# Kernel optimization log

Hardware: AMD Instinct MI355X
Metric: run time of the kernel (lower is better)

## Reference

```python
import jax, jax.numpy as jnp
import numpy as np

NUM_EXPERTS = 8
IN_FEATURES = 1024
OUT_FEATURES = 1024
TOTAL_TOKENS = 8192


def setup_inputs() -> dict:
    key = jax.random.key(0)
    k_x, k_w, k_b = jax.random.split(key, 3)
    inputs = jax.random.normal(k_x, (TOTAL_TOKENS, IN_FEATURES), dtype=jnp.float32)
    # lecun_normal-style scale for the per-expert kernels
    kernel = jax.random.normal(k_w, (NUM_EXPERTS, IN_FEATURES, OUT_FEATURES), dtype=jnp.float32) / np.sqrt(IN_FEATURES)
    bias = jax.random.normal(k_b, (NUM_EXPERTS, OUT_FEATURES), dtype=jnp.float32) * 0.01
    # ragged group sizes that sum exactly to TOTAL_TOKENS (tokens pre-sorted by expert)
    rng = np.random.default_rng(0)
    gs = rng.multinomial(TOTAL_TOKENS, [1.0 / NUM_EXPERTS] * NUM_EXPERTS)
    group_sizes = jnp.asarray(gs, dtype=jnp.int32)
    return {"inputs": inputs, "group_sizes": group_sizes, "kernel": kernel, "bias": bias}


def reference(inputs, group_sizes, kernel, bias):
    # inputs: [T, in], kernel: [E, in, out], bias: [E, out], group_sizes: [E]
    E = kernel.shape[0]
    T = inputs.shape[0]
    # per-token expert id (tokens are sorted/grouped by expert)
    expert_ids = jnp.repeat(jnp.arange(E, dtype=jnp.int32), group_sizes, total_repeat_length=T)  # [T]
    onehot = jax.nn.one_hot(expert_ids, E, dtype=inputs.dtype)  # [T, E]
    # grouped ragged matmul: y[t] = x[t] @ W[expert_ids[t]]
    xe = jnp.einsum("te,ti->eti", onehot, inputs)  # [E, T, in], zero outside each expert's group
    y = jnp.einsum("eti,eio->to", xe, kernel)  # [T, out]
    # ragged bias expansion: bias of the owning expert per token
    y = y + jnp.take(bias, expert_ids, axis=0)
    return y
```

## Files before the change

### kernel.cpp

```cpp
#include <hip/hip_runtime.h>
#include <hip/hip_bf16.h>

#define KDIM 1024
#define NDIM 1024
#define NEXP 8
#define TTOK 8192

typedef __bf16 bf16x8 __attribute__((ext_vector_type(8)));
typedef __bf16 bf16x4 __attribute__((ext_vector_type(4)));
typedef float  f32x4  __attribute__((ext_vector_type(4)));

__device__ __forceinline__ void gl2lds16(const void* g, void* l) {
  __builtin_amdgcn_global_load_lds(
      (const __attribute__((address_space(1))) void*)g,
      (__attribute__((address_space(3))) void*)l, 16, 0, 0);
}

__global__ __launch_bounds__(256) void prepass(
    const float* __restrict__ x, const float* __restrict__ W,
    __bf16* __restrict__ xb, __bf16* __restrict__ Wt)
{
  __shared__ __align__(16) __bf16 Lt[64 * 72];
  const int t = threadIdx.x;
  if (blockIdx.x < 1024) {
    int gid = blockIdx.x * 256 + t;
#pragma unroll
    for (int p = 0; p < 4; ++p) {
      size_t i8 = (size_t)(gid + p * 262144) * 8;
      float4 a = *(const float4*)(x + i8);
      float4 b = *(const float4*)(x + i8 + 4);
      bf16x8 v;
      v[0] = (__bf16)a.x; v[1] = (__bf16)a.y; v[2] = (__bf16)a.z; v[3] = (__bf16)a.w;
      v[4] = (__bf16)b.x; v[5] = (__bf16)b.y; v[6] = (__bf16)b.z; v[7] = (__bf16)b.w;
      *(bf16x8*)(xb + i8) = v;
    }
  } else {
    int bid = blockIdx.x - 1024;
    int e = bid >> 8, r = bid & 255;
    int k0 = (r >> 4) * 64, n0 = (r & 15) * 64;
    const float* Wp = W + (size_t)e * KDIM * NDIM;
    int rr0 = t >> 4, c4 = t & 15;
#pragma unroll
    for (int p = 0; p < 4; ++p) {
      int kk = rr0 + p * 16;
      float4 v = *(const float4*)(Wp + (size_t)(k0 + kk) * NDIM + n0 + c4 * 4);
      Lt[(c4 * 4 + 0) * 72 + kk] = (__bf16)v.x;
      Lt[(c4 * 4 + 1) * 72 + kk] = (__bf16)v.y;
      Lt[(c4 * 4 + 2) * 72 + kk] = (__bf16)v.z;
      Lt[(c4 * 4 + 3) * 72 + kk] = (__bf16)v.w;
    }
    __syncthreads();
    __bf16* Wte = Wt + (size_t)e * NDIM * KDIM;
    int n = t >> 2, kq = t & 3;
#pragma unroll
    for (int q = 0; q < 2; ++q) {
      int kqq = kq + q * 4;
      bf16x8 v = *(const bf16x8*)(Lt + n * 72 + kqq * 8);
      *(bf16x8*)(Wte + (size_t)(n0 + n) * KDIM + k0 + kqq * 8) = v;
    }
  }
}

__global__ __launch_bounds__(256) void moe_gemm_bf16(
    const __bf16* __restrict__ xb, const __bf16* __restrict__ Wt,
    const int* __restrict__ gs, const float* __restrict__ bias,
    float* __restrict__ out)
{
  __shared__ __align__(16) __bf16 Al0[4096], Bl0[4096];
  __shared__ __align__(16) __bf16 Al1[4096], Bl1[4096];

  int y = blockIdx.y;
  int e = 0, row0 = 0, rows = 0, found = 0, off = 0;
#pragma unroll
  for (int i = 0; i < NEXP; ++i) {
    int g = gs[i];
    int tc = (g + 127) >> 7;
    if (!found) {
      if (y < tc) { found = 1; e = i; row0 = off + y * 128; rows = min(128, g - y * 128); }
      else y -= tc;
    }
    off += g;
  }
  if (!found) return;
  const int n0 = blockIdx.x * 128;

  const int t = threadIdx.x, lane = t & 63, wv = t >> 6;
  const int wm = wv & 1, wn = wv >> 1, lm = lane & 15, lg = lane >> 4;

  const int c0 = wv * 2, c1 = wv * 2 + 1;
  const int s0 = c0 * 64 + lane, s1 = c1 * 64 + lane;
  const int r0 = s0 & 127, k0h = s0 >> 7;
  const int r1 = s1 & 127, k1h = s1 >> 7;

  const __bf16* gA0 = xb + (size_t)(row0 + r0) * KDIM + k0h * 8;
  const __bf16* gA1 = xb + (size_t)(row0 + r1) * KDIM + k1h * 8;
  const __bf16* Wte = Wt + (size_t)e * NDIM * KDIM;
  const __bf16* gB0 = Wte + (size_t)(n0 + r0) * KDIM + k0h * 8;
  const __bf16* gB1 = Wte + (size_t)(n0 + r1) * KDIM + k1h * 8;

  f32x4 acc[4][4] = {};

  auto stage = [&](int kt, __bf16* lA, __bf16* lB) {
    const int ko = kt * 32;
    gl2lds16(gA0 + ko, lA + c0 * 512);
    gl2lds16(gA1 + ko, lA + c1 * 512);
    gl2lds16(gB0 + ko, lB + c0 * 512);
    gl2lds16(gB1 + ko, lB + c1 * 512);
  };

  auto compute = [&](const __bf16* lA, const __bf16* lB) {
    bf16x8 af[4], bfr[4];
#pragma unroll
    for (int i = 0; i < 4; ++i)
      af[i] = *(const bf16x8*)(lA + lg * 1024 + (wm * 64 + i * 16 + lm) * 8);
#pragma unroll
    for (int j = 0; j < 4; ++j)
      bfr[j] = *(const bf16x8*)(lB + lg * 1024 + (wn * 64 + j * 16 + lm) * 8);
#pragma unroll
    for (int i = 0; i < 4; ++i)
#pragma unroll
      for (int j = 0; j < 4; ++j)
        acc[i][j] = __builtin_amdgcn_mfma_f32_16x16x32_bf16(af[i], bfr[j], acc[i][j], 0, 0, 0);
  };

  stage(0, Al0, Bl0);
#pragma unroll 1
  for (int kt = 0; kt < KDIM / 32; kt += 2) {
    __syncthreads();
    stage(kt + 1, Al1, Bl1);
    compute(Al0, Bl0);
    __syncthreads();
    if (kt + 2 < KDIM / 32) stage(kt + 2, Al0, Bl0);
    compute(Al1, Bl1);
  }

  float bj[4];
#pragma unroll
  for (int j = 0; j < 4; ++j) bj[j] = bias[e * NDIM + n0 + wn * 64 + j * 16 + lm];
  float* op = out + (size_t)row0 * NDIM + n0;
#pragma unroll
  for (int i = 0; i < 4; ++i)
#pragma unroll
    for (int r = 0; r < 4; ++r) {
      int rr = wm * 64 + i * 16 + lg * 4 + r;
      if (rr < rows) {
#pragma unroll
        for (int j = 0; j < 4; ++j)
          op[(size_t)rr * NDIM + wn * 64 + j * 16 + lm] = acc[i][j][r] + bj[j];
      }
    }
}

#define LDA 40
__global__ __launch_bounds__(256) void moe_gemm_kernel(
    const float* __restrict__ x, const int* __restrict__ gs,
    const float* __restrict__ W, const float* __restrict__ bias,
    float* __restrict__ out)
{
  __shared__ __bf16 Al[128 * LDA];
  __shared__ __bf16 Bl[128 * LDA];
  const int e = blockIdx.z, mt = blockIdx.y, nt = blockIdx.x;
  int off = 0;
#pragma unroll
  for (int i = 0; i < NEXP; ++i) { int g = gs[i]; if (i < e) off += g; }
  const int ge = gs[e];
  const int m0 = mt * 128;
  if (m0 >= ge) return;
  const int rows = min(128, ge - m0);
  const int row0 = off + m0;
  const int n0 = nt * 128;
  const int t = threadIdx.x, lane = t & 63, wv = t >> 6;
  const int wm = wv & 1, wn = wv >> 1, lm = lane & 15, lg = lane >> 4;
  const int am = t >> 3, kq = t & 7, nb = t & 127, kh = t >> 7;
  float4 aReg[4]; float bReg[16];
  const float* Wp = W + (size_t)e * KDIM * NDIM + n0 + nb;
  auto load_tile = [&](int kt) {
#pragma unroll
    for (int p = 0; p < 4; ++p) {
      int r = am + 32 * p;
      if (r < rows) aReg[p] = *(const float4*)(x + (size_t)(row0 + r) * KDIM + kt * 32 + kq * 4);
      else aReg[p] = make_float4(0.f, 0.f, 0.f, 0.f);
    }
    const float* wp = Wp + (size_t)(kt * 32 + kh * 16) * NDIM;
#pragma unroll
    for (int j = 0; j < 16; ++j) bReg[j] = wp[(size_t)j * NDIM];
  };
  auto store_tile = [&]() {
#pragma unroll
    for (int p = 0; p < 4; ++p) {
      bf16x4 v;
      v[0] = (__bf16)aReg[p].x; v[1] = (__bf16)aReg[p].y;
      v[2] = (__bf16)aReg[p].z; v[3] = (__bf16)aReg[p].w;
      *(bf16x4*)(Al + (am + 32 * p) * LDA + kq * 4) = v;
    }
    bf16x8 b0, b1;
#pragma unroll
    for (int j = 0; j < 8; ++j) { b0[j] = (__bf16)bReg[j]; b1[j] = (__bf16)bReg[8 + j]; }
    *(bf16x8*)(Bl + nb * LDA + kh * 16) = b0;
    *(bf16x8*)(Bl + nb * LDA + kh * 16 + 8) = b1;
  };
  f32x4 acc[4][4] = {};
  load_tile(0);
#pragma unroll 1
  for (int kt = 0; kt < KDIM / 32; ++kt) {
    __syncthreads();
    store_tile();
    __syncthreads();
    if (kt + 1 < KDIM / 32) load_tile(kt + 1);
    bf16x8 af[4], bfr[4];
#pragma unroll
    for (int i = 0; i < 4; ++i)
      af[i] = *(const bf16x8*)(Al + (wm * 64 + i * 16 + lm) * LDA + lg * 8);
#pragma unroll
    for (int j = 0; j < 4; ++j)
      bfr[j] = *(const bf16x8*)(Bl + (wn * 64 + j * 16 + lm) * LDA + lg * 8);
#pragma unroll
    for (int i = 0; i < 4; ++i)
#pragma unroll
      for (int j = 0; j < 4; ++j)
        acc[i][j] = __builtin_amdgcn_mfma_f32_16x16x32_bf16(af[i], bfr[j], acc[i][j], 0, 0, 0);
  }
  float bj[4];
#pragma unroll
  for (int j = 0; j < 4; ++j) bj[j] = bias[e * NDIM + n0 + wn * 64 + j * 16 + lm];
  float* op = out + (size_t)row0 * NDIM + n0;
#pragma unroll
  for (int i = 0; i < 4; ++i)
#pragma unroll
    for (int r = 0; r < 4; ++r) {
      int rr = wm * 64 + i * 16 + lg * 4 + r;
      if (rr < rows) {
#pragma unroll
        for (int j = 0; j < 4; ++j)
          op[(size_t)rr * NDIM + wn * 64 + j * 16 + lm] = acc[i][j][r] + bj[j];
      }
    }
}

extern "C" void kernel_launch(void* const* d_in, const int* in_sizes, int n_in,
                              void* d_out, int out_size, void* d_ws, size_t ws_size,
                              hipStream_t stream) {
  const float* x    = (const float*)d_in[0];
  const int*   gs   = (const int*)d_in[1];
  const float* W    = (const float*)d_in[2];
  const float* bias = (const float*)d_in[3];
  float*       out  = (float*)d_out;

  const size_t xb_bytes = (size_t)TTOK * KDIM * 2;
  const size_t wt_bytes = (size_t)NEXP * KDIM * NDIM * 2;
  if (ws_size >= xb_bytes + wt_bytes) {
    __bf16* xb = (__bf16*)d_ws;
    __bf16* Wt = (__bf16*)((char*)d_ws + xb_bytes);
    prepass<<<dim3(1024 + 2048), 256, 0, stream>>>(x, W, xb, Wt);
    moe_gemm_bf16<<<dim3(NDIM / 128, 72), 256, 0, stream>>>(xb, Wt, gs, bias, out);
  } else {
    moe_gemm_kernel<<<dim3(NDIM / 128, TTOK / 128, NEXP), 256, 0, stream>>>(x, gs, W, bias, out);
  }
}
```

Before: 164.4 us.

## Load MFMA fragments directly from global memory with register ring prefetch

The bf16 GEMM drops LDS staging and barriers. Each wave now loads its A and B MFMA fragments straight from global memory into a 4-deep ring of register buffers, prefetching three k-steps ahead. This removes LDS traffic and __syncthreads, but loses data sharing between waves, so each wave re-fetches rows that other waves also read. That doubles L2/global traffic and sharply raises register pressure, which may hurt occupancy or cause spills.

```diff
diff --git a/kernel.cpp b/kernel.cpp
--- a/kernel.cpp
+++ b/kernel.cpp
@@ -9,12 +9,6 @@
 typedef __bf16 bf16x8 __attribute__((ext_vector_type(8)));
 typedef __bf16 bf16x4 __attribute__((ext_vector_type(4)));
 typedef float  f32x4  __attribute__((ext_vector_type(4)));
-
-__device__ __forceinline__ void gl2lds16(const void* g, void* l) {
-  __builtin_amdgcn_global_load_lds(
-      (const __attribute__((address_space(1))) void*)g,
-      (__attribute__((address_space(3))) void*)l, 16, 0, 0);
-}
 
 __global__ __launch_bounds__(256) void prepass(
     const float* __restrict__ x, const float* __restrict__ W,
@@ -61,14 +55,11 @@
   }
 }
 
-__global__ __launch_bounds__(256) void moe_gemm_bf16(
+__global__ __launch_bounds__(256) void moe_gemm_direct(
     const __bf16* __restrict__ xb, const __bf16* __restrict__ Wt,
     const int* __restrict__ gs, const float* __restrict__ bias,
     float* __restrict__ out)
 {
-  __shared__ __align__(16) __bf16 Al0[4096], Bl0[4096];
-  __shared__ __align__(16) __bf16 Al1[4096], Bl1[4096];
-
   int y = blockIdx.y;
   int e = 0, row0 = 0, rows = 0, found = 0, off = 0;
 #pragma unroll
@@ -87,51 +78,41 @@
   const int t = threadIdx.x, lane = t & 63, wv = t >> 6;
   const int wm = wv & 1, wn = wv >> 1, lm = lane & 15, lg = lane >> 4;
 
-  const int c0 = wv * 2, c1 = wv * 2 + 1;
-  const int s0 = c0 * 64 + lane, s1 = c1 * 64 + lane;
-  const int r0 = s0 & 127, k0h = s0 >> 7;
-  const int r1 = s1 & 127, k1h = s1 >> 7;
-
-  const __bf16* gA0 = xb + (size_t)(row0 + r0) * KDIM + k0h * 8;
-  const __bf16* gA1 = xb + (size_t)(row0 + r1) * KDIM + k1h * 8;
-  const __bf16* Wte = Wt + (size_t)e * NDIM * KDIM;
-  const __bf16* gB0 = Wte + (size_t)(n0 + r0) * KDIM + k0h * 8;
-  const __bf16* gB1 = Wte + (size_t)(n0 + r1) * KDIM + k1h * 8;
+  const __bf16* aB = xb + (size_t)(row0 + wm * 64 + lm) * KDIM + lg * 8;
+  const __bf16* bB = Wt + (size_t)e * NDIM * KDIM + (size_t)(n0 + wn * 64 + lm) * KDIM + lg * 8;
 
   f32x4 acc[4][4] = {};
-
-  auto stage = [&](int kt, __bf16* lA, __bf16* lB) {
-    const int ko = kt * 32;
-    gl2lds16(gA0 + ko, lA + c0 * 512);
-    gl2lds16(gA1 + ko, lA + c1 * 512);
-    gl2lds16(gB0 + ko, lB + c0 * 512);
-    gl2lds16(gB1 + ko, lB + c1 * 512);
-  };
-
-  auto compute = [&](const __bf16* lA, const __bf16* lB) {
-    bf16x8 af[4], bfr[4];
+  bf16x8 aF[4][4], bF[4][4];
+
+  auto ld = [&](int kt, bf16x8* a, bf16x8* b) {
+    const __bf16* ap = aB + kt * 32;
+    const __bf16* bp = bB + kt * 32;
+#pragma unroll
+    for (int i = 0; i < 4; ++i) a[i] = *(const bf16x8*)(ap + (size_t)(i * 16) * KDIM);
+#pragma unroll
+    for (int j = 0; j < 4; ++j) b[j] = *(const bf16x8*)(bp + (size_t)(j * 16) * KDIM);
+  };
+  auto mm = [&](bf16x8* a, bf16x8* b) {
 #pragma unroll
     for (int i = 0; i < 4; ++i)
-      af[i] = *(const bf16x8*)(lA + lg * 1024 + (wm * 64 + i * 16 + lm) * 8);
-#pragma unroll
-    for (int j = 0; j < 4; ++j)
-      bfr[j] = *(const bf16x8*)(lB + lg * 1024 + (wn * 64 + j * 16 + lm) * 8);
-#pragma unroll
-    for (int i = 0; i < 4; ++i)
 #pragma unroll
       for (int j = 0; j < 4; ++j)
-        acc[i][j] = __builtin_amdgcn_mfma_f32_16x16x32_bf16(af[i], bfr[j], acc[i][j], 0, 0, 0);
-  };
-
-  stage(0, Al0, Bl0);
+        acc[i][j] = __builtin_amdgcn_mfma_f32_16x16x32_bf16(a[i], b[j], acc[i][j], 0, 0, 0);
+  };
+
+  ld(0, aF[0], bF[0]);
+  ld(1, aF[1], bF[1]);
+  ld(2, aF[2], bF[2]);
 #pragma unroll 1
-  for (int kt = 0; kt < KDIM / 32; kt += 2) {
-    __syncthreads();
-    stage(kt + 1, Al1, Bl1);
-    compute(Al0, Bl0);
-    __syncthreads();
-    if (kt + 2 < KDIM / 32) stage(kt + 2, Al0, Bl0);
-    compute(Al1, Bl1);
+  for (int kt = 0; kt < KDIM / 32; kt += 4) {
+    if (kt + 3 < 32) ld(kt + 3, aF[3], bF[3]);
+    mm(aF[0], bF[0]);
+    if (kt + 4 < 32) ld(kt + 4, aF[0], bF[0]);
+    mm(aF[1], bF[1]);
+    if (kt + 5 < 32) ld(kt + 5, aF[1], bF[1]);
+    mm(aF[2], bF[2]);
+    if (kt + 6 < 32) ld(kt + 6, aF[2], bF[2]);
+    mm(aF[3], bF[3]);
   }
 
   float bj[4];
@@ -252,7 +233,7 @@
     __bf16* xb = (__bf16*)d_ws;
     __bf16* Wt = (__bf16*)((char*)d_ws + xb_bytes);
     prepass<<<dim3(1024 + 2048), 256, 0, stream>>>(x, W, xb, Wt);
-    moe_gemm_bf16<<<dim3(NDIM / 128, 72), 256, 0, stream>>>(xb, Wt, gs, bias, out);
+    moe_gemm_direct<<<dim3(NDIM / 128, 72), 256, 0, stream>>>(xb, Wt, gs, bias, out);
   } else {
     moe_gemm_kernel<<<dim3(NDIM / 128, TTOK / 128, NEXP), 256, 0, stream>>>(x, gs, W, bias, out);
   }
```

Result: slower. 202.3 us (+23.0%).
